# Kernel optimization log

Measured on AMD Instinct MI355X. Metric: run time of the kernel, lower is better.

The kernel has to match this reference:

```python
import jax, jax.numpy as jnp
import numpy as np

N = 30000      # paper nodes
E = 300000     # edges per etype
IN = 128       # in_feats
HID = 128      # n_hidden
H, D = 4, 32   # n_heads, head dim (HID // H)
C = 16         # n_classes
T = 2          # n_etypes
SLOPE = 0.2    # GATConv leaky-relu negative slope


def setup_inputs() -> dict:
    key = jax.random.key(0)
    ks = jax.random.split(key, 24)
    def w(k, shape, fan):
        return jax.random.normal(k, shape, jnp.float32) * (fan ** -0.5)
    inp = {}
    inp["x"] = jax.random.normal(ks[0], (N, IN), jnp.float32)
    inp["src0"] = jax.random.randint(ks[1], (E,), 0, N, jnp.int32)
    inp["dst0"] = jax.random.randint(ks[2], (E,), 0, N, jnp.int32)
    inp["src1"] = jax.random.randint(ks[3], (E,), 0, N, jnp.int32)
    inp["dst1"] = jax.random.randint(ks[4], (E,), 0, N, jnp.int32)
    # layer 1: in_feats -> H*D, per etype (stacked on leading etype axis)
    inp["W1"]  = w(ks[5], (T, IN, H * D), IN)
    inp["al1"] = w(ks[6], (T, H, D), D)
    inp["ar1"] = w(ks[7], (T, H, D), D)
    inp["b1"]  = jnp.zeros((T, H * D), jnp.float32)
    # layers 2,3: HID -> H*D
    inp["W2"]  = w(ks[8], (T, HID, H * D), HID)
    inp["al2"] = w(ks[9], (T, H, D), D)
    inp["ar2"] = w(ks[10], (T, H, D), D)
    inp["b2"]  = jnp.zeros((T, H * D), jnp.float32)
    inp["W3"]  = w(ks[11], (T, HID, H * D), HID)
    inp["al3"] = w(ks[12], (T, H, D), D)
    inp["ar3"] = w(ks[13], (T, H, D), D)
    inp["b3"]  = jnp.zeros((T, H * D), jnp.float32)
    # output linear
    inp["Wout"] = w(ks[14], (HID, C), HID)
    inp["bout"] = jnp.zeros((C,), jnp.float32)
    return inp


def _gat(h, src, dst, W, al, ar, b):
    """Single-etype GATConv. h:[N,F], W:[F,H*D], al/ar:[H,D], b:[H*D] -> [N,H,D]."""
    feat = (h @ W).reshape(N, H, D)                       # [N,H,D]
    el = jnp.sum(feat * al, axis=-1)                      # [N,H]
    er = jnp.sum(feat * ar, axis=-1)                      # [N,H]
    e = jax.nn.leaky_relu(el[src] + er[dst], SLOPE)       # [E,H]
    # edge softmax over incoming edges of each dst node, per head
    m = jax.ops.segment_max(e, dst, num_segments=N)       # [N,H]
    ex = jnp.exp(e - m[dst])                              # [E,H]
    s = jax.ops.segment_sum(ex, dst, num_segments=N)      # [N,H]
    alpha = ex / s[dst]                                   # [E,H]
    msg = feat[src] * alpha[:, :, None]                   # [E,H,D]
    out = jax.ops.segment_sum(msg, dst, num_segments=N)   # [N,H,D]
    return out + b.reshape(1, H, D)


def _hetero_layer(h, srcs, dsts, W, al, ar, b):
    # HeteroGraphConv: sum-aggregate GATConv outputs across etypes, then flatten heads
    out = _gat(h, srcs[0], dsts[0], W[0], al[0], ar[0], b[0])
    for t in range(1, T):
        out = out + _gat(h, srcs[t], dsts[t], W[t], al[t], ar[t], b[t])
    return out.reshape(N, H * D)


def reference(x, src0, dst0, src1, dst1,
              W1, al1, ar1, b1, W2, al2, ar2, b2, W3, al3, ar3, b3,
              Wout, bout):
    srcs, dsts = (src0, src1), (dst0, dst1)
    h = _hetero_layer(x, srcs, dsts, W1, al1, ar1, b1)
    h = jax.nn.relu(h)  # dropout omitted (eval mode)
    h = _hetero_layer(h, srcs, dsts, W2, al2, ar2, b2)
    h = jax.nn.relu(h)
    h = _hetero_layer(h, srcs, dsts, W3, al3, ar3, b3)
    return h @ Wout + bout  # [N, C]
```

## Files before the change

kernel.cpp:

```cpp
#include <hip/hip_runtime.h>

#define NN 30000
#define EE 300000
#define HH 4
#define SLOPE 0.2f
#define SCAN_NB 15

typedef _Float16 f16;
typedef f16 f16x8 __attribute__((ext_vector_type(8)));
typedef float f32x4 __attribute__((ext_vector_type(4)));
typedef unsigned short u16;

__global__ __launch_bounds__(256) void prep_k(const float* __restrict__ W0,
                                              const float* __restrict__ W1,
                                              const float* __restrict__ W2,
                                              f16* __restrict__ Wh,
                                              int4* __restrict__ deg4) {
    const int z = blockIdx.z;
    if (z == 3) {
        const int base = (blockIdx.y * 8 + blockIdx.x) * 256 + threadIdx.x;
        for (int j = base; j < 2 * NN / 4; j += 4096) deg4[j] = make_int4(0, 0, 0, 0);
        return;
    }
    const int t = blockIdx.y;
    const float* W = (z == 0) ? W0 : ((z == 1) ? W1 : W2);
    f16* Whl = Wh + (size_t)z * 2 * 16384;
    const int i0 = blockIdx.x * 2048;
    #pragma unroll
    for (int j = 0; j < 8; ++j) {
        const int i = i0 + threadIdx.x + j * 256;
        const int k = i >> 7, col = i & 127;
        Whl[t * 16384 + col * 128 + k] = (f16)W[t * 16384 + i];
    }
}

#define APAD 136
__global__ __launch_bounds__(256) void gemm_mfma(const f16* __restrict__ Ah,
                                                 const float* __restrict__ Af,
                                                 const int use_f32,
                                                 const f16* __restrict__ Whbase,
                                                 const float* __restrict__ albase,
                                                 const float* __restrict__ arbase,
                                                 f16* __restrict__ featbase,
                                                 float* __restrict__ elbase,
                                                 float* __restrict__ erbase) {
    __shared__ f16 Bsl[128 * APAD];
    const int bx = blockIdx.x >> 1;
    const int et = blockIdx.x & 1;
    const f16* Wh = Whbase + et * 16384;
    f16* feat = featbase + (size_t)et * NN * 128;
    const int row0 = bx * 64;
    const int t = threadIdx.x;

    #pragma unroll
    for (int j = 0; j < 8; ++j) {
        const int idx = t + j * 256;
        const int col = idx >> 4, k16 = idx & 15;
        *reinterpret_cast<float4*>(&Bsl[col * APAD + k16 * 8]) =
            *reinterpret_cast<const float4*>(Wh + col * 128 + k16 * 8);
    }
    __syncthreads();

    const int w = t >> 6, lane = t & 63;
    const int r = lane & 15, g = lane >> 4;
    const int mb = w * 16;
    const int rowa = min(row0 + mb + r, NN - 1);
    f32x4 acc[8];
    #pragma unroll
    for (int nt = 0; nt < 8; ++nt) acc[nt] = (f32x4){0.f, 0.f, 0.f, 0.f};

    #pragma unroll
    for (int ks = 0; ks < 4; ++ks) {
        f16x8 av;
        if (use_f32) {
            const float4 a0 =
                *reinterpret_cast<const float4*>(Af + (size_t)rowa * 128 + ks * 32 + g * 8);
            const float4 a1 =
                *reinterpret_cast<const float4*>(Af + (size_t)rowa * 128 + ks * 32 + g * 8 + 4);
            av[0] = (f16)a0.x; av[1] = (f16)a0.y; av[2] = (f16)a0.z; av[3] = (f16)a0.w;
            av[4] = (f16)a1.x; av[5] = (f16)a1.y; av[6] = (f16)a1.z; av[7] = (f16)a1.w;
        } else {
            av = *reinterpret_cast<const f16x8*>(Ah + (size_t)rowa * 128 + ks * 32 + g * 8);
        }
        #pragma unroll
        for (int nt = 0; nt < 8; ++nt) {
            const f16x8 bv =
                *reinterpret_cast<const f16x8*>(&Bsl[(nt * 16 + r) * APAD + ks * 32 + g * 8]);
            acc[nt] = __builtin_amdgcn_mfma_f32_16x16x32_f16(av, bv, acc[nt], 0, 0, 0);
        }
    }

    float alv[8], arv[8];
    #pragma unroll
    for (int nt = 0; nt < 8; ++nt) {
        alv[nt] = albase[et * 128 + nt * 16 + r];
        arv[nt] = arbase[et * 128 + nt * 16 + r];
    }
    #pragma unroll
    for (int p = 0; p < 4; ++p) {
        const int row = row0 + mb + g * 4 + p;
        const bool ok = row < NN;
        if (ok) {
            #pragma unroll
            for (int nt = 0; nt < 8; ++nt)
                feat[(size_t)row * 128 + nt * 16 + r] = (f16)acc[nt][p];
        }
        #pragma unroll
        for (int h = 0; h < 4; ++h) {
            float pl = fmaf(acc[2 * h][p], alv[2 * h], acc[2 * h + 1][p] * alv[2 * h + 1]);
            float pr = fmaf(acc[2 * h][p], arv[2 * h], acc[2 * h + 1][p] * arv[2 * h + 1]);
            pl += __shfl_xor(pl, 1); pl += __shfl_xor(pl, 2);
            pl += __shfl_xor(pl, 4); pl += __shfl_xor(pl, 8);
            pr += __shfl_xor(pr, 1); pr += __shfl_xor(pr, 2);
            pr += __shfl_xor(pr, 4); pr += __shfl_xor(pr, 8);
            if (ok && r == 0) {
                elbase[et * NN * HH + row * HH + h] = pl;
                erbase[et * NN * HH + row * HH + h] = pr;
            }
        }
    }
}

__global__ __launch_bounds__(256) void hist4_k(const int* __restrict__ dst0,
                                               const int* __restrict__ dst1,
                                               int* __restrict__ deg) {
    const int i = blockIdx.x * 256 + threadIdx.x;
    if (i >= EE / 4) return;
    const int t = blockIdx.y;
    const int4 d = reinterpret_cast<const int4*>(t ? dst1 : dst0)[i];
    int* dg = deg + t * NN;
    atomicAdd(&dg[d.x], 1);
    atomicAdd(&dg[d.y], 1);
    atomicAdd(&dg[d.z], 1);
    atomicAdd(&dg[d.w], 1);
}

__global__ __launch_bounds__(256) void scan1_k(const int* __restrict__ deg,
                                               int* __restrict__ offs,
                                               int* __restrict__ blocksum) {
    const int t = blockIdx.y, b = blockIdx.x;
    const int* d = deg + t * NN;
    int* o = offs + t * (NN + 1);
    const int base = b * 2048 + threadIdx.x * 8;
    int v[8];
    int s = 0;
    #pragma unroll
    for (int j = 0; j < 8; ++j) {
        const int i = base + j;
        v[j] = (i < NN) ? d[i] : 0;
        s += v[j];
    }
    __shared__ int buf[256];
    buf[threadIdx.x] = s;
    __syncthreads();
    #pragma unroll
    for (int ofs = 1; ofs < 256; ofs <<= 1) {
        const int add = (threadIdx.x >= (unsigned)ofs) ? buf[threadIdx.x - ofs] : 0;
        __syncthreads();
        buf[threadIdx.x] += add;
        __syncthreads();
    }
    int run = buf[threadIdx.x] - s;
    #pragma unroll
    for (int j = 0; j < 8; ++j) {
        const int i = base + j;
        if (i < NN) o[i] = run;
        run += v[j];
    }
    if (threadIdx.x == 255) blocksum[t * SCAN_NB + b] = buf[255];
}

__global__ __launch_bounds__(256) void scan3b_k(int* __restrict__ offs,
                                                const int* __restrict__ blocksum,
                                                int* __restrict__ cursor) {
    const int t = blockIdx.y, b = blockIdx.x;
    int boff = 0;
    #pragma unroll
    for (int i = 0; i < SCAN_NB; ++i)
        if (i < b) boff += blocksum[t * SCAN_NB + i];
    int* o = offs + t * (NN + 1);
    int* cur = cursor + t * NN;
    if (b == SCAN_NB - 1 && threadIdx.x == 0)
        o[NN] = boff + blocksum[t * SCAN_NB + SCAN_NB - 1];
    const int base = b * 2048 + threadIdx.x * 8;
    #pragma unroll
    for (int j = 0; j < 8; ++j) {
        const int i = base + j;
        if (i < NN) {
            const int val = o[i] + boff;
            o[i] = val;
            cur[i] = val;
        }
    }
}

__global__ __launch_bounds__(256) void scatter4_k(const int* __restrict__ src0,
                                                  const int* __restrict__ dst0,
                                                  const int* __restrict__ src1,
                                                  const int* __restrict__ dst1,
                                                  int* __restrict__ cursor,
                                                  u16* __restrict__ csr_src) {
    const int i = blockIdx.x * 256 + threadIdx.x;
    if (i >= EE / 4) return;
    const int t = blockIdx.y;
    const int4 s = reinterpret_cast<const int4*>(t ? src1 : src0)[i];
    const int4 d = reinterpret_cast<const int4*>(t ? dst1 : dst0)[i];
    int* cur = cursor + t * NN;
    u16* cs = csr_src + t * EE;
    cs[atomicAdd(&cur[d.x], 1)] = (u16)s.x;
    cs[atomicAdd(&cur[d.y], 1)] = (u16)s.y;
    cs[atomicAdd(&cur[d.z], 1)] = (u16)s.z;
    cs[atomicAdd(&cur[d.w], 1)] = (u16)s.w;
}

__global__ __launch_bounds__(256) void pull_agg12_k(const u16* __restrict__ csr_src,
                                                    const int* __restrict__ offs,
                                                    const float* __restrict__ el,
                                                    const float* __restrict__ er,
                                                    const f16* __restrict__ feat,
                                                    const float* __restrict__ b0,
                                                    const float* __restrict__ b1,
                                                    f16* __restrict__ out, int relu) {
    __shared__ float xb[2][2][128];
    const int w = threadIdx.x >> 6, lane = threadIdx.x & 63;
    const int p = w >> 1, t = w & 1;
    const int n = blockIdx.x * 2 + p;
    const int sub = lane >> 4;
    const int cg = lane & 15;
    const int h = cg >> 2;
    const int c0 = cg * 8;

    const int* so = offs + t * (NN + 1);
    const int e0 = so[n], e1 = so[n + 1];

    float s = 0.f;
    float x[8];
    #pragma unroll
    for (int j = 0; j < 8; ++j) x[j] = 0.f;

    if (e0 < e1) {
        const u16* cs = csr_src + t * EE;
        const float* elt = el + t * NN * HH;
        const float erh = er[t * NN * HH + n * HH + h];
        const f16* ft = feat + (size_t)t * NN * 128;
        const int elast = e1 - 1;

        int si_0 = cs[min(e0 + sub, elast)];
        int si_1 = cs[min(e0 + 4 + sub, elast)];
        int si_2 = cs[min(e0 + 8 + sub, elast)];
        int si_3 = cs[min(e0 + 12 + sub, elast)];
        float lv_0 = elt[si_0 * HH + h];
        f16x8 fr_0 = *reinterpret_cast<const f16x8*>(ft + (size_t)si_0 * 128 + c0);
        float lv_1 = elt[si_1 * HH + h];
        f16x8 fr_1 = *reinterpret_cast<const f16x8*>(ft + (size_t)si_1 * 128 + c0);
        float lv_2 = elt[si_2 * HH + h];
        f16x8 fr_2 = *reinterpret_cast<const f16x8*>(ft + (size_t)si_2 * 128 + c0);

        for (int eb = e0; eb < e1; eb += 4) {
            const int si_4 = cs[min(eb + 16 + sub, elast)];
            const float lv_3 = elt[si_3 * HH + h];
            const f16x8 fr_3 = *reinterpret_cast<const f16x8*>(ft + (size_t)si_3 * 128 + c0);
            float v = lv_0 + erh;
            v = (v >= 0.f) ? v : v * SLOPE;
            float ex = __expf(v);
            ex = (eb + sub < e1) ? ex : 0.f;
            s += ex;
            #pragma unroll
            for (int j = 0; j < 8; ++j) x[j] = fmaf(ex, (float)fr_0[j], x[j]);
            lv_0 = lv_1; fr_0 = fr_1;
            lv_1 = lv_2; fr_1 = fr_2;
            lv_2 = lv_3; fr_2 = fr_3;
            si_3 = si_4;
        }
    }

    s += __shfl_xor(s, 16); s += __shfl_xor(s, 32);
    #pragma unroll
    for (int j = 0; j < 8; ++j) {
        x[j] += __shfl_xor(x[j], 16);
        x[j] += __shfl_xor(x[j], 32);
    }
    const float inv = (s > 0.f) ? 1.f / s : 0.f;
    if (sub == 0) {
        float4 v0 = make_float4(x[0] * inv, x[1] * inv, x[2] * inv, x[3] * inv);
        float4 v1 = make_float4(x[4] * inv, x[5] * inv, x[6] * inv, x[7] * inv);
        *reinterpret_cast<float4*>(&xb[p][t][c0]) = v0;
        *reinterpret_cast<float4*>(&xb[p][t][c0 + 4]) = v1;
    }
    __syncthreads();
    if (t == 0) {
        const int c = lane * 2;
        float a0 = xb[p][0][c] + xb[p][1][c] + b0[c] + b1[c];
        float a1 = xb[p][0][c + 1] + xb[p][1][c + 1] + b0[c + 1] + b1[c + 1];
        if (relu) { a0 = fmaxf(a0, 0.f); a1 = fmaxf(a1, 0.f); }
        union { f16 h2[2]; float f; } o;
        o.h2[0] = (f16)a0; o.h2[1] = (f16)a1;
        *reinterpret_cast<float*>(out + (size_t)n * 128 + c) = o.f;
    }
}

__global__ __launch_bounds__(256) void out_gemm_k(const f16* __restrict__ A,
                                                  const float* __restrict__ W,
                                                  const float* __restrict__ bout,
                                                  float* __restrict__ out) {
    __shared__ float At[16][132];
    const int row0 = blockIdx.x * 16;
    const int t = threadIdx.x;
    {
        const int r = t >> 4, c8 = t & 15;
        const f16x8 v = *reinterpret_cast<const f16x8*>(A + (size_t)(row0 + r) * 128 + c8 * 8);
        #pragma unroll
        for (int j = 0; j < 8; ++j) At[r][c8 * 8 + j] = (float)v[j];
    }
    __syncthreads();
    const int r = t >> 4, c = t & 15;
    float accv = 0.f;
    #pragma unroll 8
    for (int k = 0; k < 128; ++k) accv = fmaf(At[r][k], W[k * 16 + c], accv);
    out[(row0 + r) * 16 + c] = accv + bout[c];
}

extern "C" void kernel_launch(void* const* d_in, const int* in_sizes, int n_in,
                              void* d_out, int out_size, void* d_ws, size_t ws_size,
                              hipStream_t stream) {
    (void)in_sizes; (void)n_in; (void)out_size; (void)ws_size;
    const float* x = (const float*)d_in[0];
    const int* src0 = (const int*)d_in[1];
    const int* dst0 = (const int*)d_in[2];
    const int* src1 = (const int*)d_in[3];
    const int* dst1 = (const int*)d_in[4];
    const float* W[3]  = {(const float*)d_in[5], (const float*)d_in[9],  (const float*)d_in[13]};
    const float* al[3] = {(const float*)d_in[6], (const float*)d_in[10], (const float*)d_in[14]};
    const float* ar[3] = {(const float*)d_in[7], (const float*)d_in[11], (const float*)d_in[15]};
    const float* bb[3] = {(const float*)d_in[8], (const float*)d_in[12], (const float*)d_in[16]};
    const float* Wout = (const float*)d_in[17];
    const float* bout = (const float*)d_in[18];
    float* outp = (float*)d_out;

    char* pb = (char*)d_ws;
    f16* feat   = (f16*)pb;    pb += (size_t)2 * NN * 128 * 2;
    f16* hbuf   = (f16*)pb;    pb += (size_t)NN * 128 * 2;
    float* el   = (float*)pb;  pb += (size_t)2 * NN * HH * 4;
    float* er   = (float*)pb;  pb += (size_t)2 * NN * HH * 4;
    int* deg    = (int*)pb;    pb += (size_t)2 * NN * 4;
    int* cursor = (int*)pb;    pb += (size_t)2 * NN * 4;
    int* offs   = (int*)pb;    pb += (size_t)2 * (NN + 1) * 4;
    int* bsum   = (int*)pb;    pb += (size_t)2 * SCAN_NB * 4;
    f16* Wh     = (f16*)pb;    pb += (size_t)3 * 2 * 128 * 128 * 2;
    u16* csr    = (u16*)pb;    pb += (size_t)2 * EE * 2;

    prep_k<<<dim3(8, 2, 4), 256, 0, stream>>>(W[0], W[1], W[2], Wh, (int4*)deg);
    hist4_k<<<dim3((EE / 4 + 255) / 256, 2), 256, 0, stream>>>(dst0, dst1, deg);
    scan1_k<<<dim3(SCAN_NB, 2), 256, 0, stream>>>(deg, offs, bsum);
    scan3b_k<<<dim3(SCAN_NB, 2), 256, 0, stream>>>(offs, bsum, cursor);
    scatter4_k<<<dim3((EE / 4 + 255) / 256, 2), 256, 0, stream>>>(src0, dst0, src1, dst1,
                                                                  cursor, csr);

    const f16* hin = hbuf;
    for (int l = 0; l < 3; ++l) {
        gemm_mfma<<<938, 256, 0, stream>>>(
            hin, x, (l == 0) ? 1 : 0, Wh + l * 2 * 16384, al[l], ar[l], feat, el, er);
        pull_agg12_k<<<NN / 2, 256, 0, stream>>>(csr, offs, el, er, feat,
                                                 bb[l], bb[l] + 128, hbuf, (l < 2) ? 1 : 0);
        hin = hbuf;
    }
    out_gemm_k<<<NN / 16, 256, 0, stream>>>(hbuf, Wout, bout, outp);
}
```

Measured before the change: 224.0 us.

## Merge CSR scatter and layer-1 GEMM into one heterogeneous launch

The CSR scatter kernel and the first-layer feature GEMM are independent, so they now run as one launch. The first blocks do the atomic scatter of edges and the rest do the MFMA GEMM on the fp32 input. This saves one kernel launch and lets the latency-bound atomic scatter overlap with the compute-bound GEMM. The cost is a large shared-memory allocation that the scatter blocks also carry, which may reduce how many of them fit per CU.

```diff
diff --git a/kernel.cpp b/kernel.cpp
--- a/kernel.cpp
+++ b/kernel.cpp
@@ -5,6 +5,7 @@
 #define HH 4
 #define SLOPE 0.2f
 #define SCAN_NB 15
+#define SCB 293
 
 typedef _Float16 f16;
 typedef f16 f16x8 __attribute__((ext_vector_type(8)));
@@ -121,6 +122,110 @@
     }
 }
 
+__global__ __launch_bounds__(256) void gemm1_scatter_k(const float* __restrict__ Af,
+                                                       const f16* __restrict__ Whbase,
+                                                       const float* __restrict__ albase,
+                                                       const float* __restrict__ arbase,
+                                                       f16* __restrict__ featbase,
+                                                       float* __restrict__ elbase,
+                                                       float* __restrict__ erbase,
+                                                       const int* __restrict__ src0,
+                                                       const int* __restrict__ dst0,
+                                                       const int* __restrict__ src1,
+                                                       const int* __restrict__ dst1,
+                                                       int* __restrict__ cursor,
+                                                       u16* __restrict__ csr_src) {
+    __shared__ f16 Bsl[128 * APAD];
+    if (blockIdx.x < 2 * SCB) {
+        const int t = (blockIdx.x >= SCB) ? 1 : 0;
+        const int i = (blockIdx.x - t * SCB) * 256 + threadIdx.x;
+        if (i < EE / 4) {
+            const int4 s = reinterpret_cast<const int4*>(t ? src1 : src0)[i];
+            const int4 d = reinterpret_cast<const int4*>(t ? dst1 : dst0)[i];
+            int* cur = cursor + t * NN;
+            u16* cs = csr_src + t * EE;
+            cs[atomicAdd(&cur[d.x], 1)] = (u16)s.x;
+            cs[atomicAdd(&cur[d.y], 1)] = (u16)s.y;
+            cs[atomicAdd(&cur[d.z], 1)] = (u16)s.z;
+            cs[atomicAdd(&cur[d.w], 1)] = (u16)s.w;
+        }
+        return;
+    }
+    const int bxg = blockIdx.x - 2 * SCB;
+    const int bx = bxg >> 1;
+    const int et = bxg & 1;
+    const f16* Wh = Whbase + et * 16384;
+    f16* feat = featbase + (size_t)et * NN * 128;
+    const int row0 = bx * 64;
+    const int t = threadIdx.x;
+
+    #pragma unroll
+    for (int j = 0; j < 8; ++j) {
+        const int idx = t + j * 256;
+        const int col = idx >> 4, k16 = idx & 15;
+        *reinterpret_cast<float4*>(&Bsl[col * APAD + k16 * 8]) =
+            *reinterpret_cast<const float4*>(Wh + col * 128 + k16 * 8);
+    }
+    __syncthreads();
+
+    const int w = t >> 6, lane = t & 63;
+    const int r = lane & 15, g = lane >> 4;
+    const int mb = w * 16;
+    const int rowa = min(row0 + mb + r, NN - 1);
+    f32x4 acc[8];
+    #pragma unroll
+    for (int nt = 0; nt < 8; ++nt) acc[nt] = (f32x4){0.f, 0.f, 0.f, 0.f};
+
+    #pragma unroll
+    for (int ks = 0; ks < 4; ++ks) {
+        f16x8 av;
+        {
+            const float4 a0 =
+                *reinterpret_cast<const float4*>(Af + (size_t)rowa * 128 + ks * 32 + g * 8);
+            const float4 a1 =
+                *reinterpret_cast<const float4*>(Af + (size_t)rowa * 128 + ks * 32 + g * 8 + 4);
+            av[0] = (f16)a0.x; av[1] = (f16)a0.y; av[2] = (f16)a0.z; av[3] = (f16)a0.w;
+            av[4] = (f16)a1.x; av[5] = (f16)a1.y; av[6] = (f16)a1.z; av[7] = (f16)a1.w;
+        }
+        #pragma unroll
+        for (int nt = 0; nt < 8; ++nt) {
+            const f16x8 bv =
+                *reinterpret_cast<const f16x8*>(&Bsl[(nt * 16 + r) * APAD + ks * 32 + g * 8]);
+            acc[nt] = __builtin_amdgcn_mfma_f32_16x16x32_f16(av, bv, acc[nt], 0, 0, 0);
+        }
+    }
+
+    float alv[8], arv[8];
+    #pragma unroll
+    for (int nt = 0; nt < 8; ++nt) {
+        alv[nt] = albase[et * 128 + nt * 16 + r];
+        arv[nt] = arbase[et * 128 + nt * 16 + r];
+    }
+    #pragma unroll
+    for (int p = 0; p < 4; ++p) {
+        const int row = row0 + mb + g * 4 + p;
+        const bool ok = row < NN;
+        if (ok) {
+            #pragma unroll
+            for (int nt = 0; nt < 8; ++nt)
+                feat[(size_t)row * 128 + nt * 16 + r] = (f16)acc[nt][p];
+        }
+        #pragma unroll
+        for (int h = 0; h < 4; ++h) {
+            float pl = fmaf(acc[2 * h][p], alv[2 * h], acc[2 * h + 1][p] * alv[2 * h + 1]);
+            float pr = fmaf(acc[2 * h][p], arv[2 * h], acc[2 * h + 1][p] * arv[2 * h + 1]);
+            pl += __shfl_xor(pl, 1); pl += __shfl_xor(pl, 2);
+            pl += __shfl_xor(pl, 4); pl += __shfl_xor(pl, 8);
+            pr += __shfl_xor(pr, 1); pr += __shfl_xor(pr, 2);
+            pr += __shfl_xor(pr, 4); pr += __shfl_xor(pr, 8);
+            if (ok && r == 0) {
+                elbase[et * NN * HH + row * HH + h] = pl;
+                erbase[et * NN * HH + row * HH + h] = pr;
+            }
+        }
+    }
+}
+
 __global__ __launch_bounds__(256) void hist4_k(const int* __restrict__ dst0,
                                                const int* __restrict__ dst1,
                                                int* __restrict__ deg) {
@@ -192,25 +297,6 @@
             cur[i] = val;
         }
     }
-}
-
-__global__ __launch_bounds__(256) void scatter4_k(const int* __restrict__ src0,
-                                                  const int* __restrict__ dst0,
-                                                  const int* __restrict__ src1,
-                                                  const int* __restrict__ dst1,
-                                                  int* __restrict__ cursor,
-                                                  u16* __restrict__ csr_src) {
-    const int i = blockIdx.x * 256 + threadIdx.x;
-    if (i >= EE / 4) return;
-    const int t = blockIdx.y;
-    const int4 s = reinterpret_cast<const int4*>(t ? src1 : src0)[i];
-    const int4 d = reinterpret_cast<const int4*>(t ? dst1 : dst0)[i];
-    int* cur = cursor + t * NN;
-    u16* cs = csr_src + t * EE;
-    cs[atomicAdd(&cur[d.x], 1)] = (u16)s.x;
-    cs[atomicAdd(&cur[d.y], 1)] = (u16)s.y;
-    cs[atomicAdd(&cur[d.z], 1)] = (u16)s.z;
-    cs[atomicAdd(&cur[d.w], 1)] = (u16)s.w;
 }
 
 __global__ __launch_bounds__(256) void pull_agg12_k(const u16* __restrict__ csr_src,
@@ -353,16 +439,16 @@
     hist4_k<<<dim3((EE / 4 + 255) / 256, 2), 256, 0, stream>>>(dst0, dst1, deg);
     scan1_k<<<dim3(SCAN_NB, 2), 256, 0, stream>>>(deg, offs, bsum);
     scan3b_k<<<dim3(SCAN_NB, 2), 256, 0, stream>>>(offs, bsum, cursor);
-    scatter4_k<<<dim3((EE / 4 + 255) / 256, 2), 256, 0, stream>>>(src0, dst0, src1, dst1,
-                                                                  cursor, csr);
-
-    const f16* hin = hbuf;
-    for (int l = 0; l < 3; ++l) {
+    gemm1_scatter_k<<<2 * SCB + 938, 256, 0, stream>>>(x, Wh, al[0], ar[0], feat, el, er,
+                                                       src0, dst0, src1, dst1, cursor, csr);
+
+    pull_agg12_k<<<NN / 2, 256, 0, stream>>>(csr, offs, el, er, feat,
+                                             bb[0], bb[0] + 128, hbuf, 1);
+    for (int l = 1; l < 3; ++l) {
         gemm_mfma<<<938, 256, 0, stream>>>(
-            hin, x, (l == 0) ? 1 : 0, Wh + l * 2 * 16384, al[l], ar[l], feat, el, er);
+            hbuf, x, 0, Wh + l * 2 * 16384, al[l], ar[l], feat, el, er);
         pull_agg12_k<<<NN / 2, 256, 0, stream>>>(csr, offs, el, er, feat,
                                                  bb[l], bb[l] + 128, hbuf, (l < 2) ? 1 : 0);
-        hin = hbuf;
     }
     out_gemm_k<<<NN / 16, 256, 0, stream>>>(hbuf, Wout, bout, outp);
 }
```

New measurement: 221.5 us. About the same (-1.1%).
